# Kernel optimization log

Hardware: AMD Instinct MI355X
Metric: run time of the kernel (lower is better)

## Reference

```python
import jax, jax.numpy as jnp
import numpy as np

B, C, H, W = 32, 256, 32, 32
N_EMBED = 8192
BETA = 0.25  # used for the (unreturned) commitment loss in the original


def setup_inputs() -> dict:
    key = jax.random.key(0)
    k1, k2 = jax.random.split(key)
    z = jax.random.normal(k1, (B, C, H, W), dtype=jnp.float32)
    embedding = jax.random.normal(k2, (N_EMBED, C), dtype=jnp.float32)
    return {"z": z, "embedding": embedding}


def reference(z, embedding):
    # z: [b, c, h, w] -> [b, h, w, c] -> [N, d]
    b, c, h, w = z.shape
    z_bhwc = jnp.transpose(z, (0, 2, 3, 1))
    z_flat = z_bhwc.reshape(-1, c)  # [N, d]

    # Squared L2 distance to every codebook entry: [N, n_embed]
    d = (
        jnp.sum(z_flat * z_flat, axis=1, keepdims=True)
        + jnp.sum(embedding * embedding, axis=1)
        - 2.0 * jnp.einsum("nd,kd->nk", z_flat, embedding)
    )
    min_encoding_indices = jnp.argmin(d, axis=1)  # [N] int

    # Codebook gather + straight-through estimator
    z_q = embedding[min_encoding_indices].reshape(b, h, w, c)
    z_q = z_bhwc + jax.lax.stop_gradient(z_q - z_bhwc)
    z_q = jnp.transpose(z_q, (0, 3, 1, 2))  # back to [b, c, h, w]
    return z_q, min_encoding_indices
```

## Files before the change

### kernel.cpp

```cpp
#include <hip/hip_runtime.h>

#define BATCH   32
#define CDIM    256
#define HWSZ    1024
#define NTOK    32768
#define KEMB    8192
#define ZQ_SIZE (BATCH * CDIM * HWSZ)

typedef short bf16x8 __attribute__((ext_vector_type(8)));
typedef float floatx4 __attribute__((ext_vector_type(4)));

#define MSPLIT 2
#define STRIP  (KEMB / MSPLIT)
#define NCAND  (3 * MSPLIT)
#define MB8    128
#define NB8    128
#define MT8    (STRIP / MB8)

#define WS8_ESQ   0ULL
#define WS8_EQM   32768ULL
#define WS8_EH    65536ULL
#define WS8_ZH    4259840ULL
#define WS8_ZL    21037056ULL
#define WS8_PART  37814272ULL
#define WS8_IDX   39911424ULL
#define WS8_TOTAL 40042496ULL

__device__ __forceinline__ unsigned short bf16rne(float f) {
    unsigned int u = __float_as_uint(f);
    return (unsigned short)((u + 0x7fffu + ((u >> 16) & 1u)) >> 16);
}
__device__ __forceinline__ unsigned int packsplit(float f) {
    unsigned int u  = __float_as_uint(f);
    unsigned int hi = (u + 0x7fffu + ((u >> 16) & 1u)) >> 16;
    float rest      = f - __uint_as_float(hi << 16);
    unsigned int u2 = __float_as_uint(rest);
    unsigned int lo = (u2 + 0x7fffu + ((u2 >> 16) & 1u)) >> 16;
    return (hi << 16) | lo;
}
__device__ __forceinline__ unsigned umin32(unsigned a, unsigned b) { return a < b ? a : b; }
__device__ __forceinline__ unsigned umax32(unsigned a, unsigned b) { return a > b ? a : b; }

#define GLOAD_LDS16(g, l) \
    __builtin_amdgcn_global_load_lds((const __attribute__((address_space(1))) void*)(g), \
                                     (__attribute__((address_space(3))) void*)(l), 16, 0, 0)

__global__ void prep_kernel(const float* __restrict__ z, const float* __restrict__ emb,
                            float* __restrict__ eSq, float* __restrict__ eqm,
                            unsigned short* __restrict__ eh,
                            unsigned short* __restrict__ zh, unsigned short* __restrict__ zl) {
    __shared__ unsigned int tile[64][65];
    const int t = threadIdx.x;
    if (blockIdx.x < 2048) {
        int b  = blockIdx.x >> 6;
        int r  = blockIdx.x & 63;
        int dt = r >> 4, ht = r & 15;
        #pragma unroll
        for (int i = 0; i < 4; ++i) {
            int u  = t + 256 * i;
            int dr = u >> 4;
            int c4 = (u & 15) * 4;
            float4 v = *(const float4*)&z[(((size_t)(b * 256 + dt * 64 + dr)) << 10) + ht * 64 + c4];
            tile[dr][c4 + 0] = packsplit(v.x);
            tile[dr][c4 + 1] = packsplit(v.y);
            tile[dr][c4 + 2] = packsplit(v.z);
            tile[dr][c4 + 3] = packsplit(v.w);
        }
        __syncthreads();
        #pragma unroll
        for (int i = 0; i < 2; ++i) {
            int u  = t + 256 * i;
            int d8 = u & 7;
            int tr = u >> 3;
            unsigned short h8[8], l8[8];
            #pragma unroll
            for (int j = 0; j < 8; ++j) {
                unsigned int p = tile[d8 * 8 + j][tr];
                h8[j] = (unsigned short)(p >> 16);
                l8[j] = (unsigned short)(p & 0xffff);
            }
            size_t off = (size_t)(b * 1024 + ht * 64 + tr) * 256 + dt * 64 + d8 * 8;
            *(uint4*)&zh[off] = *(uint4*)h8;
            *(uint4*)&zl[off] = *(uint4*)l8;
        }
    } else {
        int k    = (blockIdx.x - 2048) * 4 + (t >> 6);
        int lane = t & 63;
        float4 v = *(const float4*)&emb[k * CDIM + lane * 4];
        float s  = v.x * v.x + v.y * v.y + v.z * v.z + v.w * v.w;
        #pragma unroll
        for (int off = 32; off; off >>= 1) s += __shfl_down(s, off);
        ushort4 h = make_ushort4(bf16rne(v.x), bf16rne(v.y), bf16rne(v.z), bf16rne(v.w));
        *(ushort4*)&eh[k * CDIM + lane * 4] = h;
        if (lane == 0) { eSq[k] = s; eqm[k] = s * 2048.0f + 8388608.0f; }
    }
}

#define EQOFF 49152u

#define ISSUE_A(rn, bo_) do { \
    const char* ga_ = gA0 + (size_t)((rn) >> 2) * 65536 + (size_t)((rn) & 3) * 128; \
    _Pragma("unroll") \
    for (int j_ = 0; j_ < 4; ++j_) \
        GLOAD_LDS16(ga_ + j_ * 4096, lds + (bo_) + wvOff + j_ * 1024); \
} while (0)

#define MFMA_ROUND(dr_, bo_) do { \
    __builtin_amdgcn_s_setprio(1); \
    _Pragma("unroll") \
    for (int dk_ = 0; dk_ < 2; ++dk_) { \
        const unsigned xoff_ = (bo_) + (((unsigned)(dk_ * 4) + (unsigned)quad) ^ cx) * 16; \
        bf16x8 afr_[4]; \
        _Pragma("unroll") \
        for (int rf_ = 0; rf_ < 4; ++rf_) afr_[rf_] = *(const bf16x8*)(lds + aR[rf_] + xoff_); \
        _Pragma("unroll") \
        for (int rf_ = 0; rf_ < 4; ++rf_) \
            _Pragma("unroll") \
            for (int cf_ = 0; cf_ < 4; ++cf_) \
                acc[rf_][cf_] = __builtin_amdgcn_mfma_f32_16x16x32_bf16(afr_[rf_], bfr[cf_][dr_][dk_], acc[rf_][cf_], 0, 0, 0); \
    } \
    __builtin_amdgcn_s_setprio(0); \
} while (0)

#define TOP3_EPI(mt_) do { \
    _Pragma("unroll") \
    for (int rf_ = 0; rf_ < 4; ++rf_) { \
        const unsigned base_ = (unsigned)((mt_) * MB8 + wm * 64 + rf_ * 16 + quad * 4); \
        floatx4 eq = *(const floatx4*)(lds + EQOFF + (base_ << 2)); \
        _Pragma("unroll") \
        for (int cf_ = 0; cf_ < 4; ++cf_) { \
            _Pragma("unroll") \
            for (int rr_ = 0; rr_ < 4; ++rr_) { \
                float kf = fmaf(acc[rf_][cf_][rr_], -4096.f, eq[rr_]); \
                unsigned key = (__float_as_uint(kf) << 12) | (base_ + (unsigned)rr_); \
                unsigned n2_, n3_; \
                asm("v_med3_u32 %0, %1, %2, %3" : "=v"(n2_) : "v"(key), "v"(k1[cf_]), "v"(k2[cf_])); \
                asm("v_med3_u32 %0, %1, %2, %3" : "=v"(n3_) : "v"(key), "v"(k2[cf_]), "v"(k3[cf_])); \
                k1[cf_] = umin32(k1[cf_], key); \
                k2[cf_] = n2_; \
                k3[cf_] = n3_; \
            } \
        } \
    } \
} while (0)

#define VMW4()  asm volatile("s_waitcnt vmcnt(4)" ::: "memory")
#define VMW0()  asm volatile("s_waitcnt vmcnt(0)" ::: "memory")
#define BARR()  asm volatile("s_barrier" ::: "memory")

__global__ __launch_bounds__(256, 2)
void dist8_kernel(const unsigned short* __restrict__ zhp,
                  const unsigned short* __restrict__ ehp,
                  const float* __restrict__ eqm,
                  uint4* __restrict__ part) {
    __shared__ __align__(16) char lds[65536];

    const int t    = threadIdx.x;
    const int lane = t & 63;
    const int wv   = t >> 6;
    const int wm   = wv >> 1, wn = wv & 1;
    const int l15  = lane & 15, quad = lane >> 4;

    const int nb = blockIdx.x & 255;
    const int q  = blockIdx.x >> 8;
    const int n0 = nb * NB8;
    const int cstrip = q * STRIP;

    const int dmaRow  = lane >> 3;
    const int dmaChnk = (lane & 7) ^ dmaRow;
    const unsigned laneGoff = (unsigned)dmaRow * 512 + (unsigned)dmaChnk * 16;

    const char* gA0 = (const char*)ehp + (size_t)(cstrip + wv * 32) * 512 + laneGoff;
    const char* gB0 = (const char*)zhp + (size_t)(n0 + wv * 32) * 512 + laneGoff;
    const unsigned wvOff = (unsigned)wv * 4096;
    const unsigned cx = (unsigned)(l15 & 7);

    bf16x8 bfr[4][4][2];

    #pragma unroll
    for (int s = 0; s < 2; ++s)
        #pragma unroll
        for (int j = 0; j < 4; ++j)
            GLOAD_LDS16(gB0 + s * 128 + j * 4096, lds + s * 16384 + wvOff + j * 1024);
    #pragma unroll
    for (int j = 0; j < 4; ++j)
        GLOAD_LDS16((const char*)(eqm + cstrip) + wv * 4096 + j * 1024 + lane * 16,
                    lds + EQOFF + (unsigned)wv * 4096 + (unsigned)j * 1024);
    __syncthreads();
    #pragma unroll
    for (int cf = 0; cf < 4; ++cf) {
        const unsigned bRow = (unsigned)(wn * 64 + cf * 16 + l15) * 128;
        #pragma unroll
        for (int s = 0; s < 2; ++s)
            #pragma unroll
            for (int dk = 0; dk < 2; ++dk)
                bfr[cf][s][dk] = *(const bf16x8*)(lds + s * 16384 + bRow +
                                    (((unsigned)(dk * 4) + (unsigned)quad) ^ cx) * 16);
    }
    __syncthreads();
    #pragma unroll
    for (int s = 0; s < 2; ++s)
        #pragma unroll
        for (int j = 0; j < 4; ++j)
            GLOAD_LDS16(gB0 + (s + 2) * 128 + j * 4096, lds + s * 16384 + wvOff + j * 1024);
    __syncthreads();
    #pragma unroll
    for (int cf = 0; cf < 4; ++cf) {
        const unsigned bRow = (unsigned)(wn * 64 + cf * 16 + l15) * 128;
        #pragma unroll
        for (int s = 0; s < 2; ++s)
            #pragma unroll
            for (int dk = 0; dk < 2; ++dk)
                bfr[cf][s + 2][dk] = *(const bf16x8*)(lds + s * 16384 + bRow +
                                    (((unsigned)(dk * 4) + (unsigned)quad) ^ cx) * 16);
    }
    __syncthreads();

    unsigned aR[4];
    #pragma unroll
    for (int rf = 0; rf < 4; ++rf) aR[rf] = (unsigned)(wm * 64 + rf * 16 + l15) * 128;

    unsigned k1[4], k2[4], k3[4];
    #pragma unroll
    for (int cf = 0; cf < 4; ++cf) { k1[cf] = 0xFFFFFFFFu; k2[cf] = 0xFFFFFFFFu; k3[cf] = 0xFFFFFFFFu; }

    ISSUE_A(0, 0u);
    ISSUE_A(1, 16384u);

    unsigned bufR = 0u;
    for (int mt = 0; mt < MT8 - 1; ++mt) {
        floatx4 acc[4][4];
        #pragma unroll
        for (int rf = 0; rf < 4; ++rf)
            #pragma unroll
            for (int cf = 0; cf < 4; ++cf) acc[rf][cf] = (floatx4){0.f, 0.f, 0.f, 0.f};

        #pragma unroll
        for (int dr = 0; dr < 4; ++dr) {
            VMW4();
            BARR();
            const unsigned bufI = (bufR == 0u) ? 32768u : bufR - 16384u;
            ISSUE_A(mt * 4 + dr + 2, bufI);
            MFMA_ROUND(dr, bufR);
            bufR = (bufR == 32768u) ? 0u : bufR + 16384u;
        }
        TOP3_EPI(mt);
    }
    {
        floatx4 acc[4][4];
        #pragma unroll
        for (int rf = 0; rf < 4; ++rf)
            #pragma unroll
            for (int cf = 0; cf < 4; ++cf) acc[rf][cf] = (floatx4){0.f, 0.f, 0.f, 0.f};

        VMW4(); BARR();
        { const unsigned bufI = (bufR == 0u) ? 32768u : bufR - 16384u; ISSUE_A(4 * MT8 - 2, bufI); }
        MFMA_ROUND(0, bufR);
        bufR = (bufR == 32768u) ? 0u : bufR + 16384u;

        VMW4(); BARR();
        { const unsigned bufI = (bufR == 0u) ? 32768u : bufR - 16384u; ISSUE_A(4 * MT8 - 1, bufI); }
        MFMA_ROUND(1, bufR);
        bufR = (bufR == 32768u) ? 0u : bufR + 16384u;

        VMW4(); BARR();
        MFMA_ROUND(2, bufR);
        bufR = (bufR == 32768u) ? 0u : bufR + 16384u;

        VMW0(); BARR();
        MFMA_ROUND(3, bufR);

        TOP3_EPI(MT8 - 1);
    }

    #pragma unroll
    for (int cf = 0; cf < 4; ++cf) {
        #pragma unroll
        for (int s = 0; s < 2; ++s) {
            int m = s ? 32 : 16;
            unsigned o1 = (unsigned)__shfl((int)k1[cf], lane ^ m, 64);
            unsigned o2 = (unsigned)__shfl((int)k2[cf], lane ^ m, 64);
            unsigned o3 = (unsigned)__shfl((int)k3[cf], lane ^ m, 64);
            unsigned a1  = umax32(k1[cf], o1);
            k1[cf]       = umin32(k1[cf], o1);
            unsigned b1  = umin32(k2[cf], o2);
            unsigned r3a = umax32(a1, b1);
            k2[cf]       = umin32(a1, b1);
            k3[cf]       = umin32(r3a, umin32(k3[cf], o3));
        }
    }

    __syncthreads();
    uint4* red = (uint4*)lds;
    if (quad == 0) {
        #pragma unroll
        for (int cf = 0; cf < 4; ++cf)
            red[wm * 128 + wn * 64 + cf * 16 + l15] = make_uint4(k1[cf], k2[cf], k3[cf], 0u);
    }
    __syncthreads();
    if (t < 128) {
        uint4 a = red[t], b = red[128 + t];
        unsigned a1  = umax32(a.x, b.x);
        unsigned r1  = umin32(a.x, b.x);
        unsigned b1  = umin32(a.y, b.y);
        unsigned r3a = umax32(a1, b1);
        unsigned r2  = umin32(a1, b1);
        unsigned r3  = umin32(r3a, umin32(a.z, b.z));
        part[q * NTOK + n0 + t] = make_uint4(r1, r2, r3, 0u);
    }
}

__global__ void rescore12_kernel(const unsigned short* __restrict__ zh,
                                 const unsigned short* __restrict__ zl,
                                 const float* __restrict__ emb,
                                 const float* __restrict__ eSq, const uint4* __restrict__ part,
                                 int* __restrict__ idx, float* __restrict__ idxF) {
    int n    = blockIdx.x * 4 + (threadIdx.x >> 6);
    int lane = threadIdx.x & 63;
    int c[NCAND];
    #pragma unroll
    for (int s = 0; s < MSPLIT; ++s) {
        uint4 p = part[s * NTOK + n];
        c[3 * s]     = s * STRIP + (int)(p.x & 0xFFFu);
        c[3 * s + 1] = s * STRIP + (int)(p.y & 0xFFFu);
        c[3 * s + 2] = s * STRIP + (int)(p.z & 0xFFFu);
    }
    ushort4 h = *(const ushort4*)&zh[(size_t)n * CDIM + lane * 4];
    ushort4 l = *(const ushort4*)&zl[(size_t)n * CDIM + lane * 4];
    float z0 = __uint_as_float((unsigned)h.x << 16) + __uint_as_float((unsigned)l.x << 16);
    float z1 = __uint_as_float((unsigned)h.y << 16) + __uint_as_float((unsigned)l.y << 16);
    float z2 = __uint_as_float((unsigned)h.z << 16) + __uint_as_float((unsigned)l.z << 16);
    float z3 = __uint_as_float((unsigned)h.w << 16) + __uint_as_float((unsigned)l.w << 16);
    float acc[NCAND];
    #pragma unroll
    for (int s = 0; s < NCAND; ++s) {
        float4 e = *(const float4*)&emb[(size_t)c[s] * CDIM + lane * 4];
        acc[s] = fmaf(z0, e.x, fmaf(z1, e.y, fmaf(z2, e.z, z3 * e.w)));
    }
    #pragma unroll
    for (int off = 32; off; off >>= 1) {
        #pragma unroll
        for (int s = 0; s < NCAND; ++s) acc[s] += __shfl_down(acc[s], off);
    }
    if (lane == 0) {
        float bd = 3.4e38f; int bi = 0x7fffffff;
        #pragma unroll
        for (int s = 0; s < NCAND; ++s) {
            float dv = eSq[c[s]] - 2.f * acc[s];
            if (dv < bd || (dv == bd && c[s] < bi)) { bd = dv; bi = c[s]; }
        }
        idx[n]  = bi;
        idxF[n] = (float)bi;
    }
}

__global__ void gather2_kernel(const float* __restrict__ emb, const int* __restrict__ idx,
                               float* __restrict__ out) {
    __shared__ float tile[32 * 260];
    __shared__ int rows[32];
    const int t  = threadIdx.x;
    const int n0 = blockIdx.x * 32;
    if (t < 32) rows[t] = idx[n0 + t];
    __syncthreads();
    {
        int r  = t >> 3;
        int c0 = (t & 7) * 32;
        const float* src = emb + (size_t)rows[r] * CDIM + c0;
        #pragma unroll
        for (int j = 0; j < 8; ++j) {
            float4 v = *(const float4*)(src + j * 4);
            *(float4*)&tile[r * 260 + c0 + j * 4] = v;
        }
    }
    __syncthreads();
    const int b   = n0 >> 10;
    const int hw0 = n0 & 1023;
    const int cg  = t >> 3;
    const int h4  = (t & 7) * 4;
    #pragma unroll
    for (int j = 0; j < 8; ++j) {
        int c = cg + j * 32;
        float4 v;
        v.x = tile[(h4 + 0) * 260 + c];
        v.y = tile[(h4 + 1) * 260 + c];
        v.z = tile[(h4 + 2) * 260 + c];
        v.w = tile[(h4 + 3) * 260 + c];
        *(float4*)&out[((size_t)b << 18) | ((size_t)c << 10) | (size_t)(hw0 + h4)] = v;
    }
}

#define F_BM  128
#define F_BK  128
#define F_BD  32
#define F_BSS (F_BK + 4)
#define F_KSPLIT 4
#define F_KPER  (KEMB / F_KSPLIT)
#define FWS_ESQ 0
#define FWS_PV  32768
#define FWS_PI  557056
#define FWS_IDX 1081344

__global__ void esq_kernel(const float* __restrict__ emb, float* __restrict__ eSq) {
    int k    = blockIdx.x * 4 + (threadIdx.x >> 6);
    int lane = threadIdx.x & 63;
    float4 v = *(const float4*)&emb[k * CDIM + lane * 4];
    float s  = v.x * v.x + v.y * v.y + v.z * v.z + v.w * v.w;
    #pragma unroll
    for (int off = 32; off; off >>= 1) s += __shfl_down(s, off);
    if (lane == 0) eSq[k] = s;
}

__global__ void dist_kernel(const float* __restrict__ z, const float* __restrict__ emb,
                            const float* __restrict__ eSq,
                            float* __restrict__ pv, int* __restrict__ pi) {
    __shared__ __align__(16) char smem[(F_BD * F_BM + F_BD * F_BSS) * 4];
    float (*As)[F_BM]  = (float (*)[F_BM])smem;
    float (*Bs)[F_BSS] = (float (*)[F_BSS])(smem + F_BD * F_BM * 4);
    const int t = threadIdx.x, tx = t & 15, ty = t >> 4;
    const int rb = blockIdx.x & 255, q = blockIdx.x >> 8;
    const int m0 = rb * F_BM, bb = m0 >> 10, hw0 = m0 & 1023;
    float minv[8]; int mini[8];
    #pragma unroll
    for (int i = 0; i < 8; ++i) { minv[i] = 3.4028235e38f; mini[i] = 0; }
    const int kbeg = q * F_KPER;
    for (int k0 = kbeg; k0 < kbeg + F_KPER; k0 += F_BK) {
        float acc[8][8];
        #pragma unroll
        for (int r = 0; r < 8; ++r)
            #pragma unroll
            for (int c = 0; c < 8; ++c) acc[r][c] = 0.f;
        for (int d0 = 0; d0 < CDIM; d0 += F_BD) {
            __syncthreads();
            #pragma unroll
            for (int i = 0; i < 4; ++i) {
                int u = t + i * 256; int m4 = (u & 31) << 2; int cR = u >> 5;
                float4 v = *(const float4*)&z[(bb << 18) + ((d0 + cR) << 10) + hw0 + m4];
                *(float4*)&As[cR][m4] = v;
            }
            #pragma unroll
            for (int i = 0; i < 4; ++i) {
                int u = t + i * 256; int kR = u >> 3; int c4 = (u & 7) << 2;
                float4 v = *(const float4*)&emb[(k0 + kR) * CDIM + d0 + c4];
                Bs[c4 + 0][kR] = v.x; Bs[c4 + 1][kR] = v.y;
                Bs[c4 + 2][kR] = v.z; Bs[c4 + 3][kR] = v.w;
            }
            __syncthreads();
            #pragma unroll
            for (int d = 0; d < F_BD; ++d) {
                float a[8], bb2[8];
                *(float4*)&a[0] = *(const float4*)&As[d][(ty << 2)];
                *(float4*)&a[4] = *(const float4*)&As[d][64 + (ty << 2)];
                *(float4*)&bb2[0] = *(const float4*)&Bs[d][(tx << 2)];
                *(float4*)&bb2[4] = *(const float4*)&Bs[d][64 + (tx << 2)];
                #pragma unroll
                for (int r = 0; r < 8; ++r)
                    #pragma unroll
                    for (int c = 0; c < 8; ++c) acc[r][c] = fmaf(a[r], bb2[c], acc[r][c]);
            }
        }
        #pragma unroll
        for (int c = 0; c < 8; ++c) {
            int kk = (c < 4) ? ((tx << 2) + c) : (64 + (tx << 2) + (c - 4));
            int kg = k0 + kk;
            float es = eSq[kg];
            #pragma unroll
            for (int r = 0; r < 8; ++r) {
                float v = fmaf(-2.f, acc[r][c], es);
                if (v < minv[r]) { minv[r] = v; mini[r] = kg; }
            }
        }
    }
    __syncthreads();
    float (*redV)[16] = (float (*)[16])smem;
    int   (*redI)[16] = (int   (*)[16])(smem + F_BM * 16 * 4);
    #pragma unroll
    for (int r = 0; r < 8; ++r) {
        int row = (r < 4) ? ((ty << 2) + r) : (64 + (ty << 2) + (r - 4));
        redV[row][tx] = minv[r]; redI[row][tx] = mini[r];
    }
    __syncthreads();
    if (t < F_BM) {
        float bv = redV[t][0]; int bi = redI[t][0];
        #pragma unroll
        for (int i = 1; i < 16; ++i) {
            float v = redV[t][i]; int ii = redI[t][i];
            if (v < bv || (v == bv && ii < bi)) { bv = v; bi = ii; }
        }
        int n = m0 + t;
        pv[q * NTOK + n] = bv; pi[q * NTOK + n] = bi;
    }
}

__global__ void merge_kernel(const float* __restrict__ pv, const int* __restrict__ pi,
                             int* __restrict__ idxOut, float* __restrict__ idxFOut) {
    int n = blockIdx.x * 256 + threadIdx.x;
    float bv = pv[n]; int bi = pi[n];
    #pragma unroll
    for (int q = 1; q < F_KSPLIT; ++q) {
        float v = pv[q * NTOK + n]; int ii = pi[q * NTOK + n];
        if (v < bv || (v == bv && ii < bi)) { bv = v; bi = ii; }
    }
    idxOut[n] = bi; idxFOut[n] = (float)bi;
}

extern "C" void kernel_launch(void* const* d_in, const int* in_sizes, int n_in,
                              void* d_out, int out_size, void* d_ws, size_t ws_size,
                              hipStream_t stream) {
    const float* z   = (const float*)d_in[0];
    const float* emb = (const float*)d_in[1];
    float* out = (float*)d_out;
    char*  ws  = (char*)d_ws;

    if (ws_size >= WS8_TOTAL) {
        float*          eSq  = (float*)(ws + WS8_ESQ);
        float*          eqm  = (float*)(ws + WS8_EQM);
        unsigned short* eh   = (unsigned short*)(ws + WS8_EH);
        unsigned short* zh   = (unsigned short*)(ws + WS8_ZH);
        unsigned short* zl   = (unsigned short*)(ws + WS8_ZL);
        uint4*          part = (uint4*)(ws + WS8_PART);
        int*            idx  = (int*)(ws + WS8_IDX);

        prep_kernel   <<<4096, 256, 0, stream>>>(z, emb, eSq, eqm, eh, zh, zl);
        dist8_kernel  <<<256 * MSPLIT, 256, 0, stream>>>(zh, eh, eqm, part);
        rescore12_kernel<<<NTOK / 4, 256, 0, stream>>>(zh, zl, emb, eSq, part, idx, out + ZQ_SIZE);
        gather2_kernel<<<NTOK / 32, 256, 0, stream>>>(emb, idx, out);
    } else {
        float* eSq = (float*)(ws + FWS_ESQ);
        float* pv  = (float*)(ws + FWS_PV);
        int*   pi  = (int*)(ws + FWS_PI);
        int*   idx = (int*)(ws + FWS_IDX);
        esq_kernel  <<<KEMB / 4, 256, 0, stream>>>(emb, eSq);
        dist_kernel <<<256 * F_KSPLIT, 256, 0, stream>>>(z, emb, eSq, pv, pi);
        merge_kernel<<<NTOK / 256, 256, 0, stream>>>(pv, pi, idx, out + ZQ_SIZE);
        gather2_kernel<<<NTOK / 32, 256, 0, stream>>>(emb, idx, out);
    }
}
```

Baseline: 249.6 us.

## Switch A-tile pipeline to two-round ping-pong halves and stream eqm per tile pair

Replaces the 3-slot rotating A buffer (one round per barrier, vmcnt(4) waits) with a 4-slot layout processed two rounds per barrier: load rounds into one half while MFMAs consume the other half. The codebook-norm (eqm) table is no longer preloaded whole into LDS. A single wave instead streams a 512-entry window into a small double-buffered region every two tiles. The goal is to halve barrier count and to shrink the eqm LDS footprint so all 64KB holds A data. Cost is LDS growth to 66KB, which may limit the 2-blocks-per-CU occupancy, and coarser waits on vmcnt(0).

```diff
diff --git a/kernel.cpp b/kernel.cpp
--- a/kernel.cpp
+++ b/kernel.cpp
@@ -96,9 +96,9 @@
     }
 }
 
-#define EQOFF 49152u
-
-#define ISSUE_A(rn, bo_) do { \
+#define EQOFF 65536u
+
+#define ISSUE_R(rn, bo_) do { \
     const char* ga_ = gA0 + (size_t)((rn) >> 2) * 65536 + (size_t)((rn) & 3) * 128; \
     _Pragma("unroll") \
     for (int j_ = 0; j_ < 4; ++j_) \
@@ -123,10 +123,12 @@
 } while (0)
 
 #define TOP3_EPI(mt_) do { \
+    const unsigned eqb_ = EQOFF + ((unsigned)(((mt_) >> 1) & 1)) * 1024u + ((unsigned)((mt_) & 1)) * 512u; \
     _Pragma("unroll") \
     for (int rf_ = 0; rf_ < 4; ++rf_) { \
-        const unsigned base_ = (unsigned)((mt_) * MB8 + wm * 64 + rf_ * 16 + quad * 4); \
-        floatx4 eq = *(const floatx4*)(lds + EQOFF + (base_ << 2)); \
+        const unsigned loc_ = (unsigned)(wm * 64 + rf_ * 16 + quad * 4); \
+        floatx4 eq = *(const floatx4*)(lds + eqb_ + (loc_ << 2)); \
+        const unsigned base_ = (unsigned)((mt_) * MB8) + loc_; \
         _Pragma("unroll") \
         for (int cf_ = 0; cf_ < 4; ++cf_) { \
             _Pragma("unroll") \
@@ -144,7 +146,6 @@
     } \
 } while (0)
 
-#define VMW4()  asm volatile("s_waitcnt vmcnt(4)" ::: "memory")
 #define VMW0()  asm volatile("s_waitcnt vmcnt(0)" ::: "memory")
 #define BARR()  asm volatile("s_barrier" ::: "memory")
 
@@ -153,7 +154,7 @@
                   const unsigned short* __restrict__ ehp,
                   const float* __restrict__ eqm,
                   uint4* __restrict__ part) {
-    __shared__ __align__(16) char lds[65536];
+    __shared__ __align__(16) char lds[67584];
 
     const int t    = threadIdx.x;
     const int lane = t & 63;
@@ -182,10 +183,12 @@
         #pragma unroll
         for (int j = 0; j < 4; ++j)
             GLOAD_LDS16(gB0 + s * 128 + j * 4096, lds + s * 16384 + wvOff + j * 1024);
-    #pragma unroll
-    for (int j = 0; j < 4; ++j)
-        GLOAD_LDS16((const char*)(eqm + cstrip) + wv * 4096 + j * 1024 + lane * 16,
-                    lds + EQOFF + (unsigned)wv * 4096 + (unsigned)j * 1024);
+    if (wv == 0) {
+        #pragma unroll
+        for (int j = 0; j < 2; ++j)
+            GLOAD_LDS16((const char*)(eqm + cstrip + j * 256) + lane * 16,
+                        lds + EQOFF + (unsigned)j * 1024u);
+    }
     __syncthreads();
     #pragma unroll
     for (int cf = 0; cf < 4; ++cf) {
@@ -224,10 +227,9 @@
     #pragma unroll
     for (int cf = 0; cf < 4; ++cf) { k1[cf] = 0xFFFFFFFFu; k2[cf] = 0xFFFFFFFFu; k3[cf] = 0xFFFFFFFFu; }
 
-    ISSUE_A(0, 0u);
-    ISSUE_A(1, 16384u);
-
-    unsigned bufR = 0u;
+    ISSUE_R(0, 0u);
+    ISSUE_R(1, 16384u);
+
     for (int mt = 0; mt < MT8 - 1; ++mt) {
         floatx4 acc[4][4];
         #pragma unroll
@@ -235,15 +237,23 @@
             #pragma unroll
             for (int cf = 0; cf < 4; ++cf) acc[rf][cf] = (floatx4){0.f, 0.f, 0.f, 0.f};
 
-        #pragma unroll
-        for (int dr = 0; dr < 4; ++dr) {
-            VMW4();
-            BARR();
-            const unsigned bufI = (bufR == 0u) ? 32768u : bufR - 16384u;
-            ISSUE_A(mt * 4 + dr + 2, bufI);
-            MFMA_ROUND(dr, bufR);
-            bufR = (bufR == 32768u) ? 0u : bufR + 16384u;
-        }
+        VMW0();
+        BARR();
+        ISSUE_R(4 * mt + 2, 32768u);
+        ISSUE_R(4 * mt + 3, 49152u);
+        if (((mt & 1) == 0) && mt >= 2 && mt <= 28 && wv == 0)
+            GLOAD_LDS16((const char*)(eqm + cstrip + (mt / 2 + 1) * 256) + lane * 16,
+                        lds + EQOFF + (unsigned)(((mt / 2 + 1) & 1)) * 1024u);
+        MFMA_ROUND(0, 0u);
+        MFMA_ROUND(1, 16384u);
+
+        VMW0();
+        BARR();
+        ISSUE_R(4 * mt + 4, 0u);
+        ISSUE_R(4 * mt + 5, 16384u);
+        MFMA_ROUND(2, 32768u);
+        MFMA_ROUND(3, 49152u);
+
         TOP3_EPI(mt);
     }
     {
@@ -253,22 +263,17 @@
             #pragma unroll
             for (int cf = 0; cf < 4; ++cf) acc[rf][cf] = (floatx4){0.f, 0.f, 0.f, 0.f};
 
-        VMW4(); BARR();
-        { const unsigned bufI = (bufR == 0u) ? 32768u : bufR - 16384u; ISSUE_A(4 * MT8 - 2, bufI); }
-        MFMA_ROUND(0, bufR);
-        bufR = (bufR == 32768u) ? 0u : bufR + 16384u;
-
-        VMW4(); BARR();
-        { const unsigned bufI = (bufR == 0u) ? 32768u : bufR - 16384u; ISSUE_A(4 * MT8 - 1, bufI); }
-        MFMA_ROUND(1, bufR);
-        bufR = (bufR == 32768u) ? 0u : bufR + 16384u;
-
-        VMW4(); BARR();
-        MFMA_ROUND(2, bufR);
-        bufR = (bufR == 32768u) ? 0u : bufR + 16384u;
-
-        VMW0(); BARR();
-        MFMA_ROUND(3, bufR);
+        VMW0();
+        BARR();
+        ISSUE_R(4 * MT8 - 2, 32768u);
+        ISSUE_R(4 * MT8 - 1, 49152u);
+        MFMA_ROUND(0, 0u);
+        MFMA_ROUND(1, 16384u);
+
+        VMW0();
+        BARR();
+        MFMA_ROUND(2, 32768u);
+        MFMA_ROUND(3, 49152u);
 
         TOP3_EPI(MT8 - 1);
     }
```

Measured after the change: 250.3 us. No clear change (+0.3%).

## Fuse rescore and gather kernels; drop setprio around MFMA rounds

Applied to the files above, without the earlier changes.

Merges the candidate rescoring kernel and the codebook gather/transpose kernel into one launch. Each block rescores 32 tokens, keeps the winning indices in shared memory, then gathers and transposes those rows into the output. This removes one kernel launch and the global index write/read round trip. Grid parallelism in the rescoring drops from 8192 blocks to 1024, each block running 8 sequential iterations. It also removes the s_setprio calls around the MFMA rounds in the distance kernel.

```diff
diff --git a/kernel.cpp b/kernel.cpp
--- a/kernel.cpp
+++ b/kernel.cpp
@@ -106,7 +106,6 @@
 } while (0)
 
 #define MFMA_ROUND(dr_, bo_) do { \
-    __builtin_amdgcn_s_setprio(1); \
     _Pragma("unroll") \
     for (int dk_ = 0; dk_ < 2; ++dk_) { \
         const unsigned xoff_ = (bo_) + (((unsigned)(dk_ * 4) + (unsigned)quad) ^ cx) * 16; \
@@ -119,7 +118,6 @@
             for (int cf_ = 0; cf_ < 4; ++cf_) \
                 acc[rf_][cf_] = __builtin_amdgcn_mfma_f32_16x16x32_bf16(afr_[rf_], bfr[cf_][dr_][dk_], acc[rf_][cf_], 0, 0, 0); \
     } \
-    __builtin_amdgcn_s_setprio(0); \
 } while (0)
 
 #define TOP3_EPI(mt_) do { \
@@ -310,47 +308,83 @@
     }
 }
 
-__global__ void rescore12_kernel(const unsigned short* __restrict__ zh,
-                                 const unsigned short* __restrict__ zl,
-                                 const float* __restrict__ emb,
-                                 const float* __restrict__ eSq, const uint4* __restrict__ part,
-                                 int* __restrict__ idx, float* __restrict__ idxF) {
-    int n    = blockIdx.x * 4 + (threadIdx.x >> 6);
-    int lane = threadIdx.x & 63;
-    int c[NCAND];
-    #pragma unroll
-    for (int s = 0; s < MSPLIT; ++s) {
-        uint4 p = part[s * NTOK + n];
-        c[3 * s]     = s * STRIP + (int)(p.x & 0xFFFu);
-        c[3 * s + 1] = s * STRIP + (int)(p.y & 0xFFFu);
-        c[3 * s + 2] = s * STRIP + (int)(p.z & 0xFFFu);
-    }
-    ushort4 h = *(const ushort4*)&zh[(size_t)n * CDIM + lane * 4];
-    ushort4 l = *(const ushort4*)&zl[(size_t)n * CDIM + lane * 4];
-    float z0 = __uint_as_float((unsigned)h.x << 16) + __uint_as_float((unsigned)l.x << 16);
-    float z1 = __uint_as_float((unsigned)h.y << 16) + __uint_as_float((unsigned)l.y << 16);
-    float z2 = __uint_as_float((unsigned)h.z << 16) + __uint_as_float((unsigned)l.z << 16);
-    float z3 = __uint_as_float((unsigned)h.w << 16) + __uint_as_float((unsigned)l.w << 16);
-    float acc[NCAND];
-    #pragma unroll
-    for (int s = 0; s < NCAND; ++s) {
-        float4 e = *(const float4*)&emb[(size_t)c[s] * CDIM + lane * 4];
-        acc[s] = fmaf(z0, e.x, fmaf(z1, e.y, fmaf(z2, e.z, z3 * e.w)));
-    }
-    #pragma unroll
-    for (int off = 32; off; off >>= 1) {
-        #pragma unroll
-        for (int s = 0; s < NCAND; ++s) acc[s] += __shfl_down(acc[s], off);
-    }
-    if (lane == 0) {
-        float bd = 3.4e38f; int bi = 0x7fffffff;
+__global__ void rescgath_kernel(const unsigned short* __restrict__ zh,
+                                const unsigned short* __restrict__ zl,
+                                const float* __restrict__ emb,
+                                const float* __restrict__ eSq, const uint4* __restrict__ part,
+                                float* __restrict__ out, float* __restrict__ idxF) {
+    __shared__ float tile[32 * 260];
+    __shared__ int rows[32];
+    const int t    = threadIdx.x;
+    const int lane = t & 63;
+    const int wv   = t >> 6;
+    const int n0   = blockIdx.x * 32;
+
+    for (int it = 0; it < 8; ++it) {
+        const int tl = it * 4 + wv;
+        const int n  = n0 + tl;
+        int c[NCAND];
+        #pragma unroll
+        for (int s = 0; s < MSPLIT; ++s) {
+            uint4 p = part[s * NTOK + n];
+            c[3 * s]     = s * STRIP + (int)(p.x & 0xFFFu);
+            c[3 * s + 1] = s * STRIP + (int)(p.y & 0xFFFu);
+            c[3 * s + 2] = s * STRIP + (int)(p.z & 0xFFFu);
+        }
+        ushort4 h = *(const ushort4*)&zh[(size_t)n * CDIM + lane * 4];
+        ushort4 l = *(const ushort4*)&zl[(size_t)n * CDIM + lane * 4];
+        float z0 = __uint_as_float((unsigned)h.x << 16) + __uint_as_float((unsigned)l.x << 16);
+        float z1 = __uint_as_float((unsigned)h.y << 16) + __uint_as_float((unsigned)l.y << 16);
+        float z2 = __uint_as_float((unsigned)h.z << 16) + __uint_as_float((unsigned)l.z << 16);
+        float z3 = __uint_as_float((unsigned)h.w << 16) + __uint_as_float((unsigned)l.w << 16);
+        float acc[NCAND];
         #pragma unroll
         for (int s = 0; s < NCAND; ++s) {
-            float dv = eSq[c[s]] - 2.f * acc[s];
-            if (dv < bd || (dv == bd && c[s] < bi)) { bd = dv; bi = c[s]; }
-        }
-        idx[n]  = bi;
-        idxF[n] = (float)bi;
+            float4 e = *(const float4*)&emb[(size_t)c[s] * CDIM + lane * 4];
+            acc[s] = fmaf(z0, e.x, fmaf(z1, e.y, fmaf(z2, e.z, z3 * e.w)));
+        }
+        #pragma unroll
+        for (int off = 32; off; off >>= 1) {
+            #pragma unroll
+            for (int s = 0; s < NCAND; ++s) acc[s] += __shfl_down(acc[s], off);
+        }
+        if (lane == 0) {
+            float bd = 3.4e38f; int bi = 0x7fffffff;
+            #pragma unroll
+            for (int s = 0; s < NCAND; ++s) {
+                float dv = eSq[c[s]] - 2.f * acc[s];
+                if (dv < bd || (dv == bd && c[s] < bi)) { bd = dv; bi = c[s]; }
+            }
+            rows[tl] = bi;
+            idxF[n]  = (float)bi;
+        }
+    }
+    __syncthreads();
+
+    {
+        int r  = t >> 3;
+        int c0 = (t & 7) * 32;
+        const float* src = emb + (size_t)rows[r] * CDIM + c0;
+        #pragma unroll
+        for (int j = 0; j < 8; ++j) {
+            float4 v = *(const float4*)(src + j * 4);
+            *(float4*)&tile[r * 260 + c0 + j * 4] = v;
+        }
+    }
+    __syncthreads();
+    const int b   = n0 >> 10;
+    const int hw0 = n0 & 1023;
+    const int cg  = t >> 3;
+    const int h4  = (t & 7) * 4;
+    #pragma unroll
+    for (int j = 0; j < 8; ++j) {
+        int c = cg + j * 32;
+        float4 v;
+        v.x = tile[(h4 + 0) * 260 + c];
+        v.y = tile[(h4 + 1) * 260 + c];
+        v.z = tile[(h4 + 2) * 260 + c];
+        v.w = tile[(h4 + 3) * 260 + c];
+        *(float4*)&out[((size_t)b << 18) | ((size_t)c << 10) | (size_t)(hw0 + h4)] = v;
     }
 }
 
@@ -518,12 +552,10 @@
         unsigned short* zh   = (unsigned short*)(ws + WS8_ZH);
         unsigned short* zl   = (unsigned short*)(ws + WS8_ZL);
         uint4*          part = (uint4*)(ws + WS8_PART);
-        int*            idx  = (int*)(ws + WS8_IDX);
 
         prep_kernel   <<<4096, 256, 0, stream>>>(z, emb, eSq, eqm, eh, zh, zl);
         dist8_kernel  <<<256 * MSPLIT, 256, 0, stream>>>(zh, eh, eqm, part);
-        rescore12_kernel<<<NTOK / 4, 256, 0, stream>>>(zh, zl, emb, eSq, part, idx, out + ZQ_SIZE);
-        gather2_kernel<<<NTOK / 32, 256, 0, stream>>>(emb, idx, out);
+        rescgath_kernel<<<NTOK / 32, 256, 0, stream>>>(zh, zl, emb, eSq, part, out, out + ZQ_SIZE);
     } else {
         float* eSq = (float*)(ws + FWS_ESQ);
         float* pv  = (float*)(ws + FWS_PV);
```

New measurement: 247.6 us. No clear change (-0.8%).
